# Kernel optimization log

Measured on AMD Instinct MI355X. Metric: run time of the kernel, lower is better.

## Reference

```python
import jax, jax.numpy as jnp
import numpy as np

N_NODES = 100000
DEG = 16
D_IN = 128
D_OUT = 128


def setup_inputs() -> dict:
    key = jax.random.key(0)
    k1, k2, k3, k4, k5, k6 = jax.random.split(key, 6)
    neighbours = jax.random.randint(k1, (N_NODES, DEG), 0, N_NODES, dtype=jnp.int64 if jax.config.jax_enable_x64 else jnp.int32)
    shape_features = jax.random.normal(k2, (N_NODES, D_IN), dtype=jnp.float32)
    scale = 1.0 / np.sqrt(D_IN)
    W1 = jax.random.normal(k3, (D_OUT, D_IN), dtype=jnp.float32) * scale
    b1 = jax.random.normal(k4, (D_OUT,), dtype=jnp.float32) * scale
    W2 = jax.random.normal(k5, (D_OUT, D_IN), dtype=jnp.float32) * scale
    b2 = jax.random.normal(k6, (D_OUT,), dtype=jnp.float32) * scale
    return {"neighbours": neighbours, "shape_features": shape_features,
            "W1": W1, "b1": b1, "W2": W2, "b2": b2}


def reference(neighbours, shape_features, W1, b1, W2, b2):
    # linear1(x): x @ W1^T + b1  -> [N, D_OUT]
    out1 = jnp.einsum('nd,od->no', shape_features, W1) + b1
    # per-node neighbor gather + sum (vectorized form of the Python loop)
    # gathered: [N, DEG, D_IN], aggr: [N, D_IN]
    aggr = shape_features[neighbours].sum(axis=1)
    out = out1 + jnp.einsum('nd,od->no', aggr, W2) + b2
    return jax.nn.relu(out)
```

## Files before the change

### kernel.cpp

```cpp
#include <hip/hip_runtime.h>
#include <hip/hip_bf16.h>
#include <stdint.h>


#define N_NODES 100000
#define DEG 16
#define KTOT 256
#define M_PAD 100096

typedef __attribute__((ext_vector_type(8))) short short8;
typedef __attribute__((ext_vector_type(4))) float floatx4;

static __device__ __forceinline__ unsigned short f2bf(float f) {
  union { float f; uint32_t u; } v; v.f = f;
  uint32_t u = v.u;
  return (unsigned short)((u + 0x7fffu + ((u >> 16) & 1u)) >> 16);
}
static __device__ __forceinline__ float bf2f(uint32_t bits16) {
  union { uint32_t u; float f; } v; v.u = bits16 << 16; return v.f;
}

__global__ __launch_bounds__(256) void k_prep(const float* __restrict__ W1, const float* __restrict__ b1,
                                              const float* __restrict__ W2, const float* __restrict__ b2,
                                              unsigned short* __restrict__ Bt, float* __restrict__ bias) {
  int t = blockIdx.x * 256 + threadIdx.x;
  int o = t >> 8, k = t & 255;
  float v = (k < 128) ? W1[o * 128 + k] : W2[o * 128 + (k - 128)];
  Bt[t] = f2bf(v);
  if (t < 128) bias[t] = b1[t] + b2[t];
}

__global__ __launch_bounds__(256) void k_convert(const float* __restrict__ x,
                                                 unsigned short* __restrict__ A) {
  int t = blockIdx.x * 256 + threadIdx.x;
  if (t >= N_NODES * 32) return;
  int n = t >> 5, c4 = t & 31;
  float4 v = *(const float4*)(x + (size_t)n * 128 + (size_t)c4 * 4);
  ushort4 o;
  o.x = f2bf(v.x); o.y = f2bf(v.y); o.z = f2bf(v.z); o.w = f2bf(v.w);
  *(ushort4*)(A + (size_t)n * 256 + (size_t)c4 * 4) = o;
}

__global__ __launch_bounds__(256) void k_aggr(const int* __restrict__ nbrs,
                                              unsigned short* __restrict__ A) {
  int gid = blockIdx.x * 4 + (threadIdx.x >> 6);
  int lane = threadIdx.x & 63;
  int myidx = nbrs[(size_t)gid * DEG + (lane & 15)];
  float a0 = 0.f, a1 = 0.f;
#pragma unroll
  for (int j = 0; j < DEG; ++j) {
    int nb = __shfl(myidx, j);
    uint32_t pv = *(const uint32_t*)(A + (size_t)nb * 256 + (size_t)lane * 2);
    a0 += bf2f(pv & 0xffffu);
    a1 += bf2f(pv >> 16);
  }
  uint32_t w = (uint32_t)f2bf(a0) | ((uint32_t)f2bf(a1) << 16);
  *(uint32_t*)(A + (size_t)gid * 256 + 128 + (size_t)lane * 2) = w;
}

__global__ __launch_bounds__(256) void k_gemm(const unsigned short* __restrict__ A,
                                              const unsigned short* __restrict__ Bt,
                                              const float* __restrict__ bias,
                                              float* __restrict__ out) {
  __shared__ unsigned short lds[16384];
  const int tid = threadIdx.x;
  const int lane = tid & 63;
  const int w = tid >> 6;
  const int wm = w >> 1, wn = w & 1;
  const size_t tile_m = (size_t)blockIdx.x * 128;

  floatx4 acc[4][4];
#pragma unroll
  for (int i = 0; i < 4; ++i)
#pragma unroll
    for (int j = 0; j < 4; ++j) acc[i][j] = (floatx4){0.f, 0.f, 0.f, 0.f};

  const int l8 = lane >> 3;
  const int slot_sw = (lane & 7) ^ l8;
  const unsigned short* Ag = A + tile_m * 256;

  for (int kt = 0; kt < 4; ++kt) {
    __syncthreads();
#pragma unroll
    for (int p = 0; p < 4; ++p) {
      int row = p * 32 + w * 8 + l8;
      const unsigned short* g = Ag + (size_t)row * 256 + kt * 64 + slot_sw * 8;
      __builtin_amdgcn_global_load_lds((const __attribute__((address_space(1))) uint32_t*)g,
                                       (__attribute__((address_space(3))) uint32_t*)&lds[(p * 4 + w) * 512],
                                       16, 0, 0);
    }
#pragma unroll
    for (int p = 0; p < 4; ++p) {
      int row = p * 32 + w * 8 + l8;
      const unsigned short* g = Bt + (size_t)row * 256 + kt * 64 + slot_sw * 8;
      __builtin_amdgcn_global_load_lds((const __attribute__((address_space(1))) uint32_t*)g,
                                       (__attribute__((address_space(3))) uint32_t*)&lds[8192 + (p * 4 + w) * 512],
                                       16, 0, 0);
    }
    __syncthreads();

#pragma unroll
    for (int ks = 0; ks < 2; ++ks) {
      short8 a[4], b[4];
      const int kb = ks * 64 + (lane >> 4) * 16;
      const int swz = (lane & 7) << 4;
#pragma unroll
      for (int mi = 0; mi < 4; ++mi) {
        int row = wm * 64 + mi * 16 + (lane & 15);
        a[mi] = *(const short8*)((const char*)lds + row * 128 + (kb ^ swz));
      }
#pragma unroll
      for (int ni = 0; ni < 4; ++ni) {
        int row = wn * 64 + ni * 16 + (lane & 15);
        b[ni] = *(const short8*)((const char*)lds + 16384 + row * 128 + (kb ^ swz));
      }
#pragma unroll
      for (int mi = 0; mi < 4; ++mi)
#pragma unroll
        for (int ni = 0; ni < 4; ++ni)
          acc[mi][ni] = __builtin_amdgcn_mfma_f32_16x16x32_bf16(a[mi], b[ni], acc[mi][ni], 0, 0, 0);
    }
  }

  float bcol[4];
#pragma unroll
  for (int ni = 0; ni < 4; ++ni) bcol[ni] = bias[wn * 64 + ni * 16 + (lane & 15)];
  const int r0 = (lane >> 4) * 4;
#pragma unroll
  for (int mi = 0; mi < 4; ++mi) {
    size_t mbase = tile_m + wm * 64 + mi * 16 + r0;
#pragma unroll
    for (int r = 0; r < 4; ++r) {
      size_t mrow = mbase + r;
      if (mrow < N_NODES) {
        float* orow = out + mrow * 128 + wn * 64 + (lane & 15);
#pragma unroll
        for (int ni = 0; ni < 4; ++ni) {
          float vv = acc[mi][ni][r] + bcol[ni];
          orow[ni * 16] = vv > 0.f ? vv : 0.f;
        }
      }
    }
  }
}

extern "C" void kernel_launch(void* const* d_in, const int* in_sizes, int n_in,
                              void* d_out, int out_size, void* d_ws, size_t ws_size,
                              hipStream_t stream) {
  const int* nbrs  = (const int*)d_in[0];
  const float* x   = (const float*)d_in[1];
  const float* W1  = (const float*)d_in[2];
  const float* b1  = (const float*)d_in[3];
  const float* W2  = (const float*)d_in[4];
  const float* b2  = (const float*)d_in[5];
  float* out = (float*)d_out;

  unsigned short* A  = (unsigned short*)d_ws;
  unsigned short* Bt = A + (size_t)M_PAD * 256;
  float* bias = (float*)(Bt + 128 * 256);

  k_prep<<<128, 256, 0, stream>>>(W1, b1, W2, b2, Bt, bias);
  k_convert<<<12500, 256, 0, stream>>>(x, A);
  k_aggr<<<25000, 256, 0, stream>>>(nbrs, A);
  k_gemm<<<782, 256, 0, stream>>>(A, Bt, bias, out);
}
```

Before: 183.2 us.

## Merge prep into convert, widen aggregation loads, triple-buffer GEMM K pipeline

Result: faster. 177.6 us (-3.0%).

```diff
diff --git a/kernel.cpp b/kernel.cpp
--- a/kernel.cpp
+++ b/kernel.cpp
@@ -1,11 +1,9 @@
 #include <hip/hip_runtime.h>
-#include <hip/hip_bf16.h>
 #include <stdint.h>
 
 
 #define N_NODES 100000
 #define DEG 16
-#define KTOT 256
 #define M_PAD 100096
 
 typedef __attribute__((ext_vector_type(8))) short short8;
@@ -20,25 +18,26 @@
   union { uint32_t u; float f; } v; v.u = bits16 << 16; return v.f;
 }
 
-__global__ __launch_bounds__(256) void k_prep(const float* __restrict__ W1, const float* __restrict__ b1,
-                                              const float* __restrict__ W2, const float* __restrict__ b2,
-                                              unsigned short* __restrict__ Bt, float* __restrict__ bias) {
-  int t = blockIdx.x * 256 + threadIdx.x;
-  int o = t >> 8, k = t & 255;
-  float v = (k < 128) ? W1[o * 128 + k] : W2[o * 128 + (k - 128)];
-  Bt[t] = f2bf(v);
-  if (t < 128) bias[t] = b1[t] + b2[t];
-}
-
 __global__ __launch_bounds__(256) void k_convert(const float* __restrict__ x,
-                                                 unsigned short* __restrict__ A) {
-  int t = blockIdx.x * 256 + threadIdx.x;
-  if (t >= N_NODES * 32) return;
-  int n = t >> 5, c4 = t & 31;
-  float4 v = *(const float4*)(x + (size_t)n * 128 + (size_t)c4 * 4);
-  ushort4 o;
-  o.x = f2bf(v.x); o.y = f2bf(v.y); o.z = f2bf(v.z); o.w = f2bf(v.w);
-  *(ushort4*)(A + (size_t)n * 256 + (size_t)c4 * 4) = o;
+                                                 unsigned short* __restrict__ A,
+                                                 const float* __restrict__ W1, const float* __restrict__ b1,
+                                                 const float* __restrict__ W2, const float* __restrict__ b2,
+                                                 unsigned short* __restrict__ Bt, float* __restrict__ bias) {
+  int b = blockIdx.x;
+  if (b < 12500) {
+    int t = b * 256 + threadIdx.x;
+    int n = t >> 5, c4 = t & 31;
+    float4 v = *(const float4*)(x + (size_t)n * 128 + (size_t)c4 * 4);
+    ushort4 o;
+    o.x = f2bf(v.x); o.y = f2bf(v.y); o.z = f2bf(v.z); o.w = f2bf(v.w);
+    *(ushort4*)(A + (size_t)n * 256 + (size_t)c4 * 4) = o;
+  } else {
+    int t = (b - 12500) * 256 + threadIdx.x;
+    int o = t >> 8, k = t & 255;
+    float v = (k < 128) ? W1[o * 128 + k] : W2[o * 128 + (k - 128)];
+    Bt[t] = f2bf(v);
+    if (t < 128) bias[t] = b1[t] + b2[t];
+  }
 }
 
 __global__ __launch_bounds__(256) void k_aggr(const int* __restrict__ nbrs,
@@ -46,28 +45,49 @@
   int gid = blockIdx.x * 4 + (threadIdx.x >> 6);
   int lane = threadIdx.x & 63;
   int myidx = nbrs[(size_t)gid * DEG + (lane & 15)];
-  float a0 = 0.f, a1 = 0.f;
+  int half = lane >> 5;
+  int c = lane & 31;
+  float a0 = 0.f, a1 = 0.f, a2 = 0.f, a3 = 0.f;
 #pragma unroll
-  for (int j = 0; j < DEG; ++j) {
-    int nb = __shfl(myidx, j);
-    uint32_t pv = *(const uint32_t*)(A + (size_t)nb * 256 + (size_t)lane * 2);
-    a0 += bf2f(pv & 0xffffu);
-    a1 += bf2f(pv >> 16);
+  for (int i = 0; i < 8; ++i) {
+    int nb = __shfl(myidx, 2 * i + half);
+    uint2 pv = *(const uint2*)(A + (size_t)nb * 256 + (size_t)c * 4);
+    a0 += bf2f(pv.x & 0xffffu); a1 += bf2f(pv.x >> 16);
+    a2 += bf2f(pv.y & 0xffffu); a3 += bf2f(pv.y >> 16);
   }
-  uint32_t w = (uint32_t)f2bf(a0) | ((uint32_t)f2bf(a1) << 16);
-  *(uint32_t*)(A + (size_t)gid * 256 + 128 + (size_t)lane * 2) = w;
+  a0 += __shfl_xor(a0, 32); a1 += __shfl_xor(a1, 32);
+  a2 += __shfl_xor(a2, 32); a3 += __shfl_xor(a3, 32);
+  if (lane < 32) {
+    uint2 w;
+    w.x = (uint32_t)f2bf(a0) | ((uint32_t)f2bf(a1) << 16);
+    w.y = (uint32_t)f2bf(a2) | ((uint32_t)f2bf(a3) << 16);
+    *(uint2*)(A + (size_t)gid * 256 + 128 + (size_t)c * 4) = w;
+  }
 }
 
-__global__ __launch_bounds__(256) void k_gemm(const unsigned short* __restrict__ A,
-                                              const unsigned short* __restrict__ Bt,
-                                              const float* __restrict__ bias,
-                                              float* __restrict__ out) {
-  __shared__ unsigned short lds[16384];
+#define VMW(n) asm volatile("s_waitcnt vmcnt(" #n ")" ::: "memory")
+#define BAR()  { asm volatile("" ::: "memory"); __builtin_amdgcn_s_barrier(); asm volatile("" ::: "memory"); }
+
+__global__ __launch_bounds__(256, 3) void k_gemm(const unsigned short* __restrict__ A,
+                                                 const unsigned short* __restrict__ Bt,
+                                                 const float* __restrict__ bias,
+                                                 float* __restrict__ out) {
+  __shared__ unsigned short lds[24576];
   const int tid = threadIdx.x;
   const int lane = tid & 63;
   const int w = tid >> 6;
   const int wm = w >> 1, wn = w & 1;
   const size_t tile_m = (size_t)blockIdx.x * 128;
+
+  float bcol[4];
+#pragma unroll
+  for (int ni = 0; ni < 4; ++ni) bcol[ni] = bias[wn * 64 + ni * 16 + (lane & 15)];
+
+  const int l4 = lane >> 2;
+  const int sw = ((lane & 3) ^ (l4 & 3)) * 16;
+  const char* Agb = (const char*)A + tile_m * 512;
+  const char* Bgb = (const char*)Bt;
+  char* ldsb = (char*)lds;
 
   floatx4 acc[4][4];
 #pragma unroll
@@ -75,56 +95,54 @@
 #pragma unroll
     for (int j = 0; j < 4; ++j) acc[i][j] = (floatx4){0.f, 0.f, 0.f, 0.f};
 
-  const int l8 = lane >> 3;
-  const int slot_sw = (lane & 7) ^ l8;
-  const unsigned short* Ag = A + tile_m * 256;
-
-  for (int kt = 0; kt < 4; ++kt) {
-    __syncthreads();
+  auto STAGE = [&](int t) {
+    char* base = ldsb + (t % 3) * 16384;
+    int ko = t * 64;
 #pragma unroll
-    for (int p = 0; p < 4; ++p) {
-      int row = p * 32 + w * 8 + l8;
-      const unsigned short* g = Ag + (size_t)row * 256 + kt * 64 + slot_sw * 8;
-      __builtin_amdgcn_global_load_lds((const __attribute__((address_space(1))) uint32_t*)g,
-                                       (__attribute__((address_space(3))) uint32_t*)&lds[(p * 4 + w) * 512],
+    for (int i = 0; i < 2; ++i) {
+      int r16 = w * 32 + i * 16;
+      const char* gA = Agb + (size_t)(r16 + l4) * 512 + ko + sw;
+      __builtin_amdgcn_global_load_lds((const __attribute__((address_space(1))) uint32_t*)gA,
+                                       (__attribute__((address_space(3))) uint32_t*)(base + r16 * 64),
+                                       16, 0, 0);
+      const char* gB = Bgb + (size_t)(r16 + l4) * 512 + ko + sw;
+      __builtin_amdgcn_global_load_lds((const __attribute__((address_space(1))) uint32_t*)gB,
+                                       (__attribute__((address_space(3))) uint32_t*)(base + 8192 + r16 * 64),
                                        16, 0, 0);
     }
+  };
+
+  auto COMPUTE = [&](int t) {
+    const char* base = ldsb + (t % 3) * 16384;
+    const int kb = (lane >> 4) * 16;
+    short8 a[4], b[4];
 #pragma unroll
-    for (int p = 0; p < 4; ++p) {
-      int row = p * 32 + w * 8 + l8;
-      const unsigned short* g = Bt + (size_t)row * 256 + kt * 64 + slot_sw * 8;
-      __builtin_amdgcn_global_load_lds((const __attribute__((address_space(1))) uint32_t*)g,
-                                       (__attribute__((address_space(3))) uint32_t*)&lds[8192 + (p * 4 + w) * 512],
-                                       16, 0, 0);
+    for (int mi = 0; mi < 4; ++mi) {
+      int row = wm * 64 + mi * 16 + (lane & 15);
+      a[mi] = *(const short8*)(base + row * 64 + (kb ^ ((row & 3) << 4)));
     }
-    __syncthreads();
+#pragma unroll
+    for (int ni = 0; ni < 4; ++ni) {
+      int row = wn * 64 + ni * 16 + (lane & 15);
+      b[ni] = *(const short8*)(base + 8192 + row * 64 + (kb ^ ((row & 3) << 4)));
+    }
+#pragma unroll
+    for (int mi = 0; mi < 4; ++mi)
+#pragma unroll
+      for (int ni = 0; ni < 4; ++ni)
+        acc[mi][ni] = __builtin_amdgcn_mfma_f32_16x16x32_bf16(a[mi], b[ni], acc[mi][ni], 0, 0, 0);
+  };
 
-#pragma unroll
-    for (int ks = 0; ks < 2; ++ks) {
-      short8 a[4], b[4];
-      const int kb = ks * 64 + (lane >> 4) * 16;
-      const int swz = (lane & 7) << 4;
-#pragma unroll
-      for (int mi = 0; mi < 4; ++mi) {
-        int row = wm * 64 + mi * 16 + (lane & 15);
-        a[mi] = *(const short8*)((const char*)lds + row * 128 + (kb ^ swz));
-      }
-#pragma unroll
-      for (int ni = 0; ni < 4; ++ni) {
-        int row = wn * 64 + ni * 16 + (lane & 15);
-        b[ni] = *(const short8*)((const char*)lds + 16384 + row * 128 + (kb ^ swz));
-      }
-#pragma unroll
-      for (int mi = 0; mi < 4; ++mi)
-#pragma unroll
-        for (int ni = 0; ni < 4; ++ni)
-          acc[mi][ni] = __builtin_amdgcn_mfma_f32_16x16x32_bf16(a[mi], b[ni], acc[mi][ni], 0, 0, 0);
-    }
-  }
+  STAGE(0); STAGE(1); STAGE(2);
+  VMW(8); BAR(); COMPUTE(0); BAR(); STAGE(3);
+  VMW(8); BAR(); COMPUTE(1); BAR(); STAGE(4);
+  VMW(8); BAR(); COMPUTE(2); BAR(); STAGE(5);
+  VMW(8); BAR(); COMPUTE(3); BAR(); STAGE(6);
+  VMW(8); BAR(); COMPUTE(4); BAR(); STAGE(7);
+  VMW(8); BAR(); COMPUTE(5); BAR();
+  VMW(4); BAR(); COMPUTE(6); BAR();
+  VMW(0); BAR(); COMPUTE(7);
 
-  float bcol[4];
-#pragma unroll
-  for (int ni = 0; ni < 4; ++ni) bcol[ni] = bias[wn * 64 + ni * 16 + (lane & 15)];
   const int r0 = (lane >> 4) * 4;
 #pragma unroll
   for (int mi = 0; mi < 4; ++mi) {
@@ -159,8 +177,7 @@
   unsigned short* Bt = A + (size_t)M_PAD * 256;
   float* bias = (float*)(Bt + 128 * 256);
 
-  k_prep<<<128, 256, 0, stream>>>(W1, b1, W2, b2, Bt, bias);
-  k_convert<<<12500, 256, 0, stream>>>(x, A);
+  k_convert<<<12628, 256, 0, stream>>>(x, A, W1, b1, W2, b2, Bt, bias);
   k_aggr<<<25000, 256, 0, stream>>>(nbrs, A);
   k_gemm<<<782, 256, 0, stream>>>(A, Bt, bias, out);
 }
```
